# Performance work log

Measured on AMD Instinct MI355X. Metric: run time of the kernel, lower is better.

Reference implementation:

```python
import jax, jax.numpy as jnp
import numpy as np

TEMP = 0.07
BASE_TEMP = 0.07
EPS = 1e-8


def setup_inputs() -> dict:
    key = jax.random.key(0)
    features = jax.random.normal(key, (4096, 2, 128), dtype=jnp.float32)
    return {"features": features}


def reference(features):
    B, V, D = features.shape  # bsz, n_views, dim
    # torch.cat(torch.unbind(features, dim=1), dim=0): view-major ordering
    cf = jnp.swapaxes(features, 0, 1).reshape(V * B, D)  # [N, D], N = V*B
    # cosine similarity = normalize rows then GEMM (same math as broadcasted CosineSimilarity)
    n = cf / jnp.maximum(jnp.linalg.norm(cf, axis=-1, keepdims=True), EPS)
    logits = jnp.matmul(n, n.T) / TEMP  # [N, N]
    N = V * B
    logits_mask = 1.0 - jnp.eye(N, dtype=logits.dtype)  # zero out self-contrast
    # SimCLR mask: eye(B) tiled over (anchor_count, contrast_count), minus diagonal
    pos_mask = jnp.tile(jnp.eye(B, dtype=logits.dtype), (V, V)) * logits_mask
    exp_logits = jnp.exp(logits) * logits_mask
    log_prob = logits - jnp.log(exp_logits.sum(axis=1, keepdims=True))
    mean_log_prob_pos = (pos_mask * log_prob).sum(axis=1) / pos_mask.sum(axis=1)
    loss = -(TEMP / BASE_TEMP) * mean_log_prob_pos
    return loss.reshape(V, B).mean()
```

## Files before the change

kernel.cpp:

```cpp
#include <hip/hip_runtime.h>
#include <hip/hip_bf16.h>
#include <math.h>


constexpr int   Bsz   = 4096;
constexpr int   Nrows = 8192;
constexpr int   Dd    = 128;
constexpr float TEMPf = 0.07f;
constexpr float EPSN  = 1e-8f;
constexpr float SCALE = 1.4426950408889634f / 0.07f;
constexpr float LN2   = 0.6931471805599453f;

constexpr int CHUNKS     = 32;
constexpr int CHUNK_COLS = Nrows / CHUNKS;
constexpr int TILES      = CHUNK_COLS / 32;
constexpr int ROWS_BLK   = 256;
constexpr int YG         = Nrows / ROWS_BLK;
constexpr int PREPBLKS   = Bsz / 4;

typedef __attribute__((ext_vector_type(8)))  short bf16x8;
typedef __attribute__((ext_vector_type(16))) float floatx16;


constexpr size_t OFF_PART = 0x200000;
constexpr size_t OFF_SPOS = 0x300000;

__device__ __forceinline__ void gld_lds16(const void* g, void* l) {
    __builtin_amdgcn_global_load_lds(
        (const __attribute__((address_space(1))) void*)g,
        (__attribute__((address_space(3))) void*)l, 16, 0, 0);
}

__global__ void prep_k(const float* __restrict__ f,
                       char* __restrict__ nF,
                       float* __restrict__ sposPart,
                       float* __restrict__ out) {
    __shared__ float sred[4];
    int tid  = threadIdx.x;
    int wid  = tid >> 6;
    int lane = tid & 63;
    int b    = blockIdx.x * 4 + wid;
    if (blockIdx.x == 0 && tid == 0) out[0] = 0.f;

    const float* s0 = f + (size_t)(b * 2) * Dd;
    float2 x = *(const float2*)(s0 + lane * 2);
    float2 y = *(const float2*)(s0 + Dd + lane * 2);
    float ss0 = x.x * x.x + x.y * x.y;
    float ss1 = y.x * y.x + y.y * y.y;
    float dt  = x.x * y.x + x.y * y.y;
    #pragma unroll
    for (int off = 32; off; off >>= 1) {
        ss0 += __shfl_xor(ss0, off);
        ss1 += __shfl_xor(ss1, off);
        dt  += __shfl_xor(dt,  off);
    }
    float inv0 = 1.0f / fmaxf(sqrtf(ss0), EPSN);
    float inv1 = 1.0f / fmaxf(sqrtf(ss1), EPSN);

    size_t poff = (size_t)(lane >> 3) * 1024 + ((lane >> 2) & 1) * 512
                + (lane & 3) * 4;

    __hip_bfloat162 h;
    h.x = __float2bfloat16(x.x * inv0);
    h.y = __float2bfloat16(x.y * inv0);
    *(__hip_bfloat162*)(nF + (size_t)(b >> 5) * 8192 + (b & 31) * 16 + poff) = h;
    int r1 = Bsz + b;
    h.x = __float2bfloat16(y.x * inv1);
    h.y = __float2bfloat16(y.y * inv1);
    *(__hip_bfloat162*)(nF + (size_t)(r1 >> 5) * 8192 + (r1 & 31) * 16 + poff) = h;

    if (lane == 0) sred[wid] = dt * inv0 * inv1 / TEMPf;
    __syncthreads();
    if (tid == 0) sposPart[blockIdx.x] = sred[0] + sred[1] + sred[2] + sred[3];
}

__global__ __launch_bounds__(256, 3)
void main_k(const char* __restrict__ nF, float* __restrict__ partial) {
    __shared__ char  bufs[2][8192];
    __shared__ float colred[4][256];
    const int tid  = threadIdx.x;
    const int wid  = tid >> 6;
    const int lane = tid & 63;
    const int lo   = lane & 31;
    const int hi   = lane >> 5;
    const int gy   = blockIdx.y;
    const int rbase = gy * ROWS_BLK + wid * 64;
    const int cbase = blockIdx.x * CHUNK_COLS;
    const int cg0   = cbase >> 5;

    bf16x8 afrag[2][8];
    #pragma unroll
    for (int s = 0; s < 2; s++) {
        const char* ag = nF + (size_t)((rbase + s * 32) >> 5) * 8192 + lane * 16;
        #pragma unroll
        for (int kc = 0; kc < 8; kc++)
            afrag[s][kc] = *(const bf16x8*)(ag + kc * 1024);
    }

    {
        const char* g0 = nF + (size_t)cg0 * 8192;
        int kc = wid * 2;
        gld_lds16(g0 + kc * 1024 + lane * 16,       &bufs[0][kc * 1024]);
        gld_lds16(g0 + (kc + 1) * 1024 + lane * 16, &bufs[0][(kc + 1) * 1024]);
    }

    floatx16 zero = {};

    #pragma unroll 1
    for (int t = 0; t < TILES; t++) {
        __syncthreads();
        if (t + 1 < TILES) {
            const char* gn = nF + (size_t)(cg0 + t + 1) * 8192;
            char* dst = bufs[(t + 1) & 1];
            int kc = wid * 2;
            gld_lds16(gn + kc * 1024 + lane * 16,       dst + kc * 1024);
            gld_lds16(gn + (kc + 1) * 1024 + lane * 16, dst + (kc + 1) * 1024);
        }

        const char* buf = bufs[t & 1];
        floatx16 acc0 = zero, acc1 = zero;
        #pragma unroll
        for (int kc = 0; kc < 8; kc++) {
            bf16x8 bf = *(const bf16x8*)&buf[kc * 1024 + lane * 16];
            acc0 = __builtin_amdgcn_mfma_f32_32x32x16_bf16(afrag[0][kc], bf, acc0, 0, 0, 0);
            acc1 = __builtin_amdgcn_mfma_f32_32x32x16_bf16(afrag[1][kc], bf, acc1, 0, 0, 0);
        }

        const int cb32 = cbase + t * 32;
        float cs = 0.f;
        #pragma unroll
        for (int s = 0; s < 2; s++) {
            const floatx16& acc = s ? acc1 : acc0;
            if (cb32 == rbase + s * 32) {
                #pragma unroll
                for (int r = 0; r < 16; r++) {
                    float e = __builtin_amdgcn_exp2f(acc[r] * SCALE);
                    if (lo == ((r & 3) + 8 * (r >> 2) + 4 * hi)) e = 0.f;
                    cs += e;
                }
            } else {
                #pragma unroll
                for (int r = 0; r < 16; r++)
                    cs += __builtin_amdgcn_exp2f(acc[r] * SCALE);
            }
        }
        cs += __shfl_xor(cs, 32);
        if (hi == 0) colred[wid][t * 32 + lo] = cs;
    }

    __syncthreads();
    float v = colred[0][tid] + colred[1][tid] + colred[2][tid] + colred[3][tid];
    partial[(size_t)gy * Nrows + cbase + tid] = v;
}

__global__ __launch_bounds__(256)
void final_k(const float* __restrict__ partial, const float* __restrict__ sposPart,
             float* __restrict__ out) {
    __shared__ float red[4];
    int tid = threadIdx.x;
    int r = blockIdx.x * 256 + tid;
    float se = 0.f;
    #pragma unroll
    for (int p = 0; p < YG; p++) se += partial[(size_t)p * Nrows + r];
    float acc = __builtin_amdgcn_logf(se) * LN2;
    if (tid < 32) acc -= 2.f * sposPart[blockIdx.x * 32 + tid];
    #pragma unroll
    for (int off = 32; off; off >>= 1) acc += __shfl_xor(acc, off);
    if ((tid & 63) == 0) red[tid >> 6] = acc;
    __syncthreads();
    if (tid == 0)
        atomicAdd(out, (red[0] + red[1] + red[2] + red[3]) / (float)Nrows);
}

extern "C" void kernel_launch(void* const* d_in, const int* in_sizes, int n_in,
                              void* d_out, int out_size, void* d_ws, size_t ws_size,
                              hipStream_t stream) {
    const float* f = (const float*)d_in[0];
    char* ws = (char*)d_ws;
    char* nF        = ws;
    float* partial  = (float*)(ws + OFF_PART);
    float* sposPart = (float*)(ws + OFF_SPOS);

    prep_k<<<PREPBLKS, 256, 0, stream>>>(f, nF, sposPart, (float*)d_out);
    dim3 grid(CHUNKS, YG);
    main_k<<<grid, 256, 0, stream>>>(nF, partial);
    final_k<<<Nrows / 256, 256, 0, stream>>>(partial, sposPart, (float*)d_out);
}
```

Baseline: 79.47 us.

## Exploit Gram matrix symmetry by computing only upper-triangular block pairs

Because the similarity matrix is symmetric, the main kernel now launches one block per upper-triangular pair of 256-row chunks. Each off-diagonal block contributes its exp sums both as column sums and as row sums, which roughly halves the MFMA and exp work. LDS double buffering via global_load_lds is replaced with register double-buffered direct global loads. Occupancy is lowered to 2 blocks per CU, and the added row-sum registers and shuffle reductions raise register pressure.

```diff
diff --git a/kernel.cpp b/kernel.cpp
--- a/kernel.cpp
+++ b/kernel.cpp
@@ -15,6 +15,7 @@
 constexpr int CHUNK_COLS = Nrows / CHUNKS;
 constexpr int TILES      = CHUNK_COLS / 32;
 constexpr int ROWS_BLK   = 256;
+constexpr int NPAIRS     = CHUNKS * (CHUNKS + 1) / 2;
 constexpr int YG         = Nrows / ROWS_BLK;
 constexpr int PREPBLKS   = Bsz / 4;
 
@@ -24,12 +25,6 @@
 
 constexpr size_t OFF_PART = 0x200000;
 constexpr size_t OFF_SPOS = 0x300000;
-
-__device__ __forceinline__ void gld_lds16(const void* g, void* l) {
-    __builtin_amdgcn_global_load_lds(
-        (const __attribute__((address_space(1))) void*)g,
-        (__attribute__((address_space(3))) void*)l, 16, 0, 0);
-}
 
 __global__ void prep_k(const float* __restrict__ f,
                        char* __restrict__ nF,
@@ -74,19 +69,30 @@
     if (tid == 0) sposPart[blockIdx.x] = sred[0] + sred[1] + sred[2] + sred[3];
 }
 
-__global__ __launch_bounds__(256, 3)
+__device__ __forceinline__ void load_tile(bf16x8* dst, const char* gB, int t,
+                                          int lane) {
+    #pragma unroll
+    for (int kc = 0; kc < 8; kc++)
+        dst[kc] = *(const bf16x8*)(gB + (size_t)t * 8192 + kc * 1024 + lane * 16);
+}
+
+__global__ __launch_bounds__(256, 2)
 void main_k(const char* __restrict__ nF, float* __restrict__ partial) {
-    __shared__ char  bufs[2][8192];
     __shared__ float colred[4][256];
+    __shared__ float rred[256];
     const int tid  = threadIdx.x;
     const int wid  = tid >> 6;
     const int lane = tid & 63;
     const int lo   = lane & 31;
     const int hi   = lane >> 5;
-    const int gy   = blockIdx.y;
-    const int rbase = gy * ROWS_BLK + wid * 64;
-    const int cbase = blockIdx.x * CHUNK_COLS;
-    const int cg0   = cbase >> 5;
+
+    int p = blockIdx.x, ci = 0;
+    while (p >= CHUNKS - ci) { p -= CHUNKS - ci; ci++; }
+    const int cj = ci + p;
+
+    const int rbase = ci * ROWS_BLK + wid * 64;
+    const int cbase = cj * ROWS_BLK;
+    const char* gB  = nF + (size_t)(cj * 8) * 8192;
 
     bf16x8 afrag[2][8];
     #pragma unroll
@@ -97,35 +103,19 @@
             afrag[s][kc] = *(const bf16x8*)(ag + kc * 1024);
     }
 
-    {
-        const char* g0 = nF + (size_t)cg0 * 8192;
-        int kc = wid * 2;
-        gld_lds16(g0 + kc * 1024 + lane * 16,       &bufs[0][kc * 1024]);
-        gld_lds16(g0 + (kc + 1) * 1024 + lane * 16, &bufs[0][(kc + 1) * 1024]);
-    }
-
-    floatx16 zero = {};
-
-    #pragma unroll 1
-    for (int t = 0; t < TILES; t++) {
-        __syncthreads();
-        if (t + 1 < TILES) {
-            const char* gn = nF + (size_t)(cg0 + t + 1) * 8192;
-            char* dst = bufs[(t + 1) & 1];
-            int kc = wid * 2;
-            gld_lds16(gn + kc * 1024 + lane * 16,       dst + kc * 1024);
-            gld_lds16(gn + (kc + 1) * 1024 + lane * 16, dst + (kc + 1) * 1024);
+    float rs[2][16];
+    #pragma unroll
+    for (int s = 0; s < 2; s++)
+        #pragma unroll
+        for (int r = 0; r < 16; r++) rs[s][r] = 0.f;
+
+    auto compute = [&](const bf16x8 (&bf)[8], int t) {
+        floatx16 acc0 = {}, acc1 = {};
+        #pragma unroll
+        for (int kc = 0; kc < 8; kc++) {
+            acc0 = __builtin_amdgcn_mfma_f32_32x32x16_bf16(afrag[0][kc], bf[kc], acc0, 0, 0, 0);
+            acc1 = __builtin_amdgcn_mfma_f32_32x32x16_bf16(afrag[1][kc], bf[kc], acc1, 0, 0, 0);
         }
-
-        const char* buf = bufs[t & 1];
-        floatx16 acc0 = zero, acc1 = zero;
-        #pragma unroll
-        for (int kc = 0; kc < 8; kc++) {
-            bf16x8 bf = *(const bf16x8*)&buf[kc * 1024 + lane * 16];
-            acc0 = __builtin_amdgcn_mfma_f32_32x32x16_bf16(afrag[0][kc], bf, acc0, 0, 0, 0);
-            acc1 = __builtin_amdgcn_mfma_f32_32x32x16_bf16(afrag[1][kc], bf, acc1, 0, 0, 0);
-        }
-
         const int cb32 = cbase + t * 32;
         float cs = 0.f;
         #pragma unroll
@@ -136,21 +126,52 @@
                 for (int r = 0; r < 16; r++) {
                     float e = __builtin_amdgcn_exp2f(acc[r] * SCALE);
                     if (lo == ((r & 3) + 8 * (r >> 2) + 4 * hi)) e = 0.f;
-                    cs += e;
+                    cs += e; rs[s][r] += e;
                 }
             } else {
                 #pragma unroll
-                for (int r = 0; r < 16; r++)
-                    cs += __builtin_amdgcn_exp2f(acc[r] * SCALE);
+                for (int r = 0; r < 16; r++) {
+                    float e = __builtin_amdgcn_exp2f(acc[r] * SCALE);
+                    cs += e; rs[s][r] += e;
+                }
             }
         }
         cs += __shfl_xor(cs, 32);
         if (hi == 0) colred[wid][t * 32 + lo] = cs;
+    };
+
+    bf16x8 bA[8], bB[8];
+    load_tile(bA, gB, 0, lane);
+    #pragma unroll 1
+    for (int t = 0; t < TILES; t += 2) {
+        load_tile(bB, gB, t + 1, lane);
+        compute(bA, t);
+        if (t + 2 < TILES) load_tile(bA, gB, t + 2, lane);
+        compute(bB, t + 1);
+    }
+
+    if (ci != cj) {
+        #pragma unroll
+        for (int s = 0; s < 2; s++) {
+            #pragma unroll
+            for (int r = 0; r < 16; r++) {
+                float v = rs[s][r];
+                v += __shfl_xor(v, 1);
+                v += __shfl_xor(v, 2);
+                v += __shfl_xor(v, 4);
+                v += __shfl_xor(v, 8);
+                v += __shfl_xor(v, 16);
+                if (lo == r)
+                    rred[wid * 64 + s * 32 + ((r & 3) + 8 * (r >> 2) + 4 * hi)] = v;
+            }
+        }
     }
 
     __syncthreads();
     float v = colred[0][tid] + colred[1][tid] + colred[2][tid] + colred[3][tid];
-    partial[(size_t)gy * Nrows + cbase + tid] = v;
+    partial[(size_t)ci * Nrows + cbase + tid] = v;
+    if (ci != cj)
+        partial[(size_t)cj * Nrows + ci * ROWS_BLK + tid] = rred[tid];
 }
 
 __global__ __launch_bounds__(256)
@@ -182,7 +203,6 @@
     float* sposPart = (float*)(ws + OFF_SPOS);
 
     prep_k<<<PREPBLKS, 256, 0, stream>>>(f, nF, sposPart, (float*)d_out);
-    dim3 grid(CHUNKS, YG);
-    main_k<<<grid, 256, 0, stream>>>(nF, partial);
+    main_k<<<NPAIRS, 256, 0, stream>>>(nF, partial);
     final_k<<<Nrows / 256, 256, 0, stream>>>(partial, sposPart, (float*)d_out);
 }
```

Measured after the change: 87.05 us. 1.1x slower.
